# Optimization experiments

Measured on AMD Instinct MI355X. Metric: run time of the kernel, lower is better.

The kernel has to match this reference:

```python
import jax, jax.numpy as jnp
import numpy as np

B, T, C = 16, 1024, 1024
H = 4          # wshare
K = 31         # kernel_size


def setup_inputs() -> dict:
    key = jax.random.key(0)
    ks = jax.random.split(key, 8)
    s = 1.0 / np.sqrt(C)
    return {
        "query": jax.random.normal(ks[0], (B, T, C), jnp.float32),
        "key_t": jax.random.normal(ks[1], (B, T, C), jnp.float32),   # unused, API compat
        "value": jax.random.normal(ks[2], (B, T, C), jnp.float32),   # unused, API compat
        "mask": jnp.ones((B, 1, T), jnp.int32),
        "W1": jax.random.uniform(ks[3], (2 * C, C), jnp.float32, -s, s),
        "b1": jnp.zeros((2 * C,), jnp.float32),
        "W2": jax.random.uniform(ks[4], (C, C), jnp.float32, -s, s),
        "b2": jnp.zeros((C,), jnp.float32),
        "conv_w": jax.random.uniform(ks[5], (H, K), jnp.float32, 0.0, 1.0),
        "bias": jnp.zeros((C,), jnp.float32),
    }


def reference(query, key_t, value, mask, W1, b1, W2, b2, conv_w, bias):
    # linear1 + GLU: (B,T,C) -> (B,T,2C) -> (B,T,C)
    x = query @ W1.T + b1
    a, g = jnp.split(x, 2, axis=-1)
    x = a * jax.nn.sigmoid(g)
    # (B,T,C) -> (B,C,T) -> (B*C/H, H, T); channel c uses shared kernel c % H
    x = jnp.transpose(x, (0, 2, 1)).reshape(B * C // H, H, T)
    # softmax-normalized shared kernels (H,K); dropout_rate=0 (eval)
    w = jax.nn.softmax(conv_w, axis=-1)
    y = jax.lax.conv_general_dilated(
        x, w[:, None, :], window_strides=(1,), padding=[(K // 2, K // 2)],
        feature_group_count=H, dimension_numbers=("NCH", "OIH", "NCH"))
    x = y.reshape(B, C, T) + bias[None, :, None]
    x = jnp.transpose(x, (0, 2, 1))               # (B,T,C)
    # padding mask: (B,1,T) -> transpose(-1,-2) -> (B,T,1), zero masked frames
    m = jnp.transpose(mask, (0, 2, 1))
    x = jnp.where(m == 0, 0.0, x)
    return x @ W2.T + b2
```

## Files before the change

kernel.cpp:

```cpp
#include <hip/hip_runtime.h>

typedef __attribute__((ext_vector_type(8))) __bf16 bf16x8;
typedef __attribute__((ext_vector_type(4))) __bf16 bf16x4;
typedef __attribute__((ext_vector_type(4))) float  f32x4;
typedef __attribute__((ext_vector_type(4))) float  float4v;

#define DEV static __device__ __forceinline__

DEV void gload_lds16(const void* g, void* l) {
  __builtin_amdgcn_global_load_lds(
      (const __attribute__((address_space(1))) void*)g,
      (__attribute__((address_space(3))) void*)l, 16, 0, 0);
}

__global__ void prep_all_kernel(const float* __restrict__ q, const float* __restrict__ W1,
                                const float* __restrict__ W2, const float* __restrict__ cw,
                                const float* __restrict__ b1,
                                __bf16* __restrict__ qb, __bf16* __restrict__ w1p,
                                __bf16* __restrict__ w2b,
                                float* __restrict__ swm, float* __restrict__ b1p) {
  const int blk = blockIdx.x;
  const int tid = threadIdx.x;
  if (blk < 2048) {
    int i = blk * 256 + tid;
#pragma unroll 8
    for (int it = 0; it < 8; ++it, i += 524288) {
      float4v v = ((const float4v*)q)[i];
      bf16x4 o;
#pragma unroll
      for (int j = 0; j < 4; ++j) o[j] = (__bf16)v[j];
      ((bf16x4*)qb)[i] = o;
    }
  } else if (blk < 3072) {
    const int r   = (blk - 2048) * 2 + (tid >> 7);
    const int col = (tid & 127) * 8;
    const int g  = r >> 8, p = r & 255;
    const int wn = p >> 6, jj = (p >> 4) & 3, c16 = p & 15;
    const int ch = g * 128 + wn * 32 + (jj & 1) * 16 + c16;
    const int src = ch + (jj >= 2 ? 1024 : 0);
    const float* ptr = W1 + (long)src * 1024 + col;
    float4v v0 = *(const float4v*)ptr;
    float4v v1 = *(const float4v*)(ptr + 4);
    bf16x8 o;
#pragma unroll
    for (int j = 0; j < 4; ++j) { o[j] = (__bf16)v0[j]; o[4 + j] = (__bf16)v1[j]; }
    *(bf16x8*)(w1p + (long)r * 1024 + col) = o;
  } else if (blk < 3328) {
    int i = (blk - 3072) * 256 + tid;
#pragma unroll 4
    for (int it = 0; it < 4; ++it, i += 65536) {
      float4v v = ((const float4v*)W2)[i];
      bf16x4 o;
#pragma unroll
      for (int j = 0; j < 4; ++j) o[j] = (__bf16)v[j];
      ((bf16x4*)w2b)[i] = o;
    }
  } else {
    if (tid < 4) {
      const int h = tid;
      float m = cw[h * 31];
#pragma unroll
      for (int k = 1; k < 31; ++k) m = fmaxf(m, cw[h * 31 + k]);
      float e[31];
      float s = 0.f;
#pragma unroll
      for (int k = 0; k < 31; ++k) {
        e[k] = __expf(cw[h * 31 + k] - m);
        s += e[k];
      }
      float inv = 1.f / s;
#pragma unroll
      for (int k = 0; k < 31; ++k) swm[h * 31 + k] = e[k] * inv;
    }
    for (int i = tid; i < 2048; i += 256) {
      const int g = i >> 8, p = i & 255;
      const int wn = p >> 6, jj = (p >> 4) & 3, c16 = p & 15;
      const int ch = g * 128 + wn * 32 + (jj & 1) * 16 + c16;
      b1p[i] = b1[ch + (jj >= 2 ? 1024 : 0)];
    }
  }
}

template <int MODE>
DEV void gemm_body(const __bf16* __restrict__ A, const __bf16* __restrict__ Bw,
                   const float* __restrict__ bias, void* __restrict__ Cout,
                   int M, int N, int K, int ntn) {
  __shared__ __align__(16) __bf16 Al[3 * 16384];
  __shared__ __align__(16) __bf16 Bl[2 * 16384];

  const int tid  = threadIdx.x;
  const int lane = tid & 63;
  const int w    = tid >> 6;
  const int wm = w >> 2, wn = w & 3;

  const int nwg = gridDim.x;
  const int cpx = nwg >> 3;
  const int bid = blockIdx.x;
  const int wgid = (bid & 7) * cpx + (bid >> 3);
  const int m0 = (wgid / ntn) * 256;
  const int n0 = (wgid % ntn) * 256;

  const int NT = K >> 6;

  const int scolE = ((((tid & 7) * 16) ^ (((tid >> 3) & 7) << 4)) >> 1);
  const __bf16* __restrict__ Abase = A + (long)m0 * K;
  const __bf16* __restrict__ Bbase = Bw + (long)n0 * K;

  const int l15 = lane & 15;
  const int xk  = (l15 & 7) << 4;
  const int a0  = l15 * 128 + (((lane >> 4) * 16) ^ xk);
  const int a1  = l15 * 128 + ((((lane >> 4) * 16) + 64) ^ xk);
  const int bq  = (wn & 1) * 8192;
  const int b0  = bq + a0;
  const int b1r = bq + a1;

  f32x4 acc[8][4];
#pragma unroll
  for (int i = 0; i < 8; ++i)
#pragma unroll
    for (int j = 0; j < 4; ++j) {
      acc[i][j][0] = 0.f; acc[i][j][1] = 0.f;
      acc[i][j][2] = 0.f; acc[i][j][3] = 0.f;
    }
  bf16x8 af[8], bf[8];

#define STAGEG(base, groff, ktc, dst)                                             \
  {                                                                               \
    const __bf16* _s = (base) + (long)((groff) + (tid >> 3)) * K + (ktc) + scolE; \
    gload_lds16(_s, (dst) + tid * 8);                                             \
    gload_lds16(_s + (long)64 * K, (dst) + 4096 + tid * 8);                       \
  }

#define PH_MID()                                     \
  __builtin_amdgcn_s_barrier();                      \
  asm volatile("s_waitcnt lgkmcnt(0)" ::: "memory"); \
  __builtin_amdgcn_s_setprio(1);

#define PH_ENDN()                                    \
  __builtin_amdgcn_s_setprio(0);                     \
  __builtin_amdgcn_s_barrier();

#define PH_END4()                                    \
  __builtin_amdgcn_s_setprio(0);                     \
  asm volatile("s_waitcnt vmcnt(4)" ::: "memory");   \
  __builtin_amdgcn_s_barrier();

#define RDA(IB, G)                                                    \
  _Pragma("unroll") for (int i2 = 0; i2 < 4; ++i2) {                  \
    af[i2 * 2 + 0] = *(const bf16x8*)((G) + ((IB) + i2) * 2048 + a0); \
    af[i2 * 2 + 1] = *(const bf16x8*)((G) + ((IB) + i2) * 2048 + a1); \
  }
#define RDB(JB, G)                                                                \
  _Pragma("unroll") for (int j2 = 0; j2 < 2; ++j2) {                              \
    bf[(JB) * 2 + j2 * 2 + 0] = *(const bf16x8*)((G) + ((JB) + j2) * 2048 + b0);  \
    bf[(JB) * 2 + j2 * 2 + 1] = *(const bf16x8*)((G) + ((JB) + j2) * 2048 + b1r); \
  }

#define MMQ(IB, JB)                                                           \
  _Pragma("unroll") for (int i2 = 0; i2 < 4; ++i2)                            \
  _Pragma("unroll") for (int j2 = 0; j2 < 2; ++j2)                            \
  _Pragma("unroll") for (int kk = 0; kk < 2; ++kk)                            \
      acc[(IB) + i2][(JB) + j2] = __builtin_amdgcn_mfma_f32_16x16x32_bf16(    \
          af[i2 * 2 + kk], bf[(JB) * 2 + j2 * 2 + kk], acc[(IB) + i2][(JB) + j2], 0, 0, 0);

  __bf16* aRd = Al;
  __bf16* aNx = Al + 16384;
  __bf16* aSt = Al + 32768;
  __bf16* bRd = Bl;
  __bf16* bSt = Bl + 16384;

  STAGEG(Abase, 0,   0, aRd);
  STAGEG(Abase, 128, 0, aRd + 8192);
  STAGEG(Bbase, 0,   0, bRd);
  STAGEG(Bbase, 128, 0, bRd + 8192);
  {
    const int k1 = (1 < NT ? 1 : NT - 1) * 64;
    STAGEG(Abase, 0,   k1, aNx);
    STAGEG(Abase, 128, k1, aNx + 8192);
  }
  asm volatile("s_waitcnt vmcnt(4)" ::: "memory");
  __builtin_amdgcn_s_barrier();

#pragma unroll 1
  for (int t = 0; t < NT; ++t) {
    const int kB = ((t + 1 < NT) ? t + 1 : NT - 1) * 64;
    const int kA = ((t + 2 < NT) ? t + 2 : NT - 1) * 64;
    const char* aG = (const char*)aRd + wm * 16384;
    const char* bG = (const char*)bRd + (wn >> 1) * 16384;
    RDA(0, aG); RDB(0, bG);
    STAGEG(Bbase, 0,   kB, bSt);
    STAGEG(Bbase, 128, kB, bSt + 8192);
    PH_MID(); MMQ(0, 0); PH_ENDN();
    RDB(2, bG);
    STAGEG(Abase, 0,   kA, aSt);
    STAGEG(Abase, 128, kA, aSt + 8192);
    PH_MID(); MMQ(0, 2); PH_ENDN();
    RDA(4, aG);
    PH_MID(); MMQ(4, 0); PH_ENDN();
    PH_MID(); MMQ(4, 2); PH_END4();
    __bf16* ta = aRd; aRd = aNx; aNx = aSt; aSt = ta;
    __bf16* tb = bRd; bRd = bSt; bSt = tb;
  }

  asm volatile("s_waitcnt vmcnt(0)" ::: "memory");

  const int crow = (lane >> 4) * 4;
  const int ccol = lane & 15;
  if (MODE == 0) {
    __builtin_amdgcn_s_barrier();
    float* wa = (float*)Al + w * 1088;
    const int rr = lane >> 4;
    const int cf = (lane & 15) * 4;
#pragma unroll
    for (int i = 0; i < 8; ++i) {
#pragma unroll
      for (int j = 0; j < 4; ++j) {
        const int ncol = n0 + wn * 64 + j * 16 + ccol;
        const float bv = bias[ncol];
#pragma unroll
        for (int r = 0; r < 4; ++r)
          wa[(crow + r) * 68 + j * 16 + ccol] = acc[i][j][r] + bv;
      }
#pragma unroll
      for (int s = 0; s < 4; ++s) {
        const int row = s * 4 + rr;
        const int gr = m0 + wm * 128 + i * 16 + row;
        *(float4v*)((float*)Cout + (long)gr * N + n0 + wn * 64 + cf) =
            *(const f32x4*)(wa + row * 68 + cf);
      }
    }
  } else {
    __builtin_amdgcn_s_barrier();
    __bf16* wa = (__bf16*)Al + w * 640;
    const int chbase = (n0 >> 1) + wn * 32;
    const int rr = lane >> 2, c8 = (lane & 3) * 8;
#pragma unroll
    for (int i = 0; i < 8; ++i) {
#pragma unroll
      for (int j = 0; j < 2; ++j) {
        const int na = n0 + wn * 64 + j * 16 + ccol;
        const float bva = bias[na];
        const float bvg = bias[na + 32];
#pragma unroll
        for (int r = 0; r < 4; ++r) {
          float a = acc[i][j][r] + bva;
          float gv = acc[i][j + 2][r] + bvg;
          float res = a * __builtin_amdgcn_rcpf(1.f + __expf(-gv));
          wa[(crow + r) * 40 + j * 16 + ccol] = (__bf16)res;
        }
      }
      bf16x8 v = *(const bf16x8*)(wa + rr * 40 + c8);
      const int gr = m0 + wm * 128 + i * 16 + rr;
      *(bf16x8*)((__bf16*)Cout + (long)gr * (N >> 1) + chbase + c8) = v;
    }
  }
#undef STAGEG
#undef PH_MID
#undef PH_ENDN
#undef PH_END4
#undef RDA
#undef RDB
#undef MMQ
}

__global__ __launch_bounds__(512, 1)
void gemm1_glu_kernel(const __bf16* __restrict__ A, const __bf16* __restrict__ Bw,
                      const float* __restrict__ bias, void* __restrict__ Cout,
                      int M, int N, int K, int ntn) {
  gemm_body<1>(A, Bw, bias, Cout, M, N, K, ntn);
}

__global__ __launch_bounds__(512, 1)
void gemm2_out_kernel(const __bf16* __restrict__ A, const __bf16* __restrict__ Bw,
                      const float* __restrict__ bias, void* __restrict__ Cout,
                      int M, int N, int K, int ntn) {
  gemm_body<0>(A, Bw, bias, Cout, M, N, K, ntn);
}

__global__ __launch_bounds__(256, 2)
void conv_kernel(const __bf16* __restrict__ Yin, const float* __restrict__ Wsm,
                 const float* __restrict__ bias, const int* __restrict__ mask,
                 __bf16* __restrict__ Y) {
  const int b  = blockIdx.z;
  const int t0 = blockIdx.y * 64;
  const int c0 = blockIdx.x * 128;
  __shared__ float sgT[128][128];
  __shared__ float swl[124];
  const int tid = threadIdx.x;
  if (tid < 124) swl[tid] = Wsm[tid];

  for (int i = tid; i < 2048; i += 256) {
    const int ttl = i & 127;
    const int cg  = i >> 7;
    if (ttl < 94) {
      const int t = t0 - 15 + ttl;
      float v[8];
      if (t >= 0 && t < 1024) {
        bf16x8 a8 = *(const bf16x8*)(Yin + ((long)(b * 1024 + t)) * 1024 + c0 + cg * 8);
#pragma unroll
        for (int j = 0; j < 8; ++j) v[j] = (float)a8[j];
      } else {
#pragma unroll
        for (int j = 0; j < 8; ++j) v[j] = 0.f;
      }
      const int q = ttl >> 2, e = ttl & 3;
#pragma unroll
      for (int j = 0; j < 8; ++j) {
        const int c = cg * 8 + j;
        sgT[c][((q ^ ((c & 7) << 2)) << 2) + e] = v[j];
      }
    }
  }
  __syncthreads();

  const int cc = tid & 127;
  const int th = tid >> 7;
  const int c  = c0 + cc;
  const float* wrow = swl + (c & 3) * 31;
  const float bv = bias[c];
  float acc[32];
#pragma unroll
  for (int u = 0; u < 32; ++u) acc[u] = bv;
  const int key = (cc & 7) << 2;
#pragma unroll
  for (int qi = 0; qi < 16; ++qi) {
    const int q = th * 8 + qi;
    const f32x4 w4 = *(const f32x4*)&sgT[cc][(q ^ key) << 2];
#pragma unroll
    for (int j = 0; j < 4; ++j) {
      const int rl = qi * 4 + j;
#pragma unroll
      for (int u = 0; u < 32; ++u) {
        const int k = rl - u;
        if (k >= 0 && k < 31) acc[u] += w4[j] * wrow[k];
      }
    }
  }
  const long yb = (long)b * 1024 * 1024;
#pragma unroll
  for (int u = 0; u < 32; ++u) {
    const int gt = t0 + th * 32 + u;
    float v = acc[u];
    if (mask[b * 1024 + gt] == 0) v = 0.f;
    Y[yb + (long)gt * 1024 + c] = (__bf16)v;
  }
}

extern "C" void kernel_launch(void* const* d_in, const int* in_sizes, int n_in,
                              void* d_out, int out_size, void* d_ws, size_t ws_size,
                              hipStream_t stream) {
  const float* q    = (const float*)d_in[0];
  const int*   mask = (const int*)d_in[3];
  const float* W1   = (const float*)d_in[4];
  const float* b1   = (const float*)d_in[5];
  const float* W2   = (const float*)d_in[6];
  const float* b2   = (const float*)d_in[7];
  const float* cw   = (const float*)d_in[8];
  const float* bias = (const float*)d_in[9];

  char* ws = (char*)d_ws;
  __bf16* q_bf  = (__bf16*)(ws);
  __bf16* w1p   = (__bf16*)(ws + (32u << 20));
  __bf16* w2_bf = (__bf16*)(ws + (36u << 20));
  float*  swm   = (float*)(ws + (38u << 20));
  float*  b1p   = (float*)(ws + (38u << 20) + 4096);
  __bf16* y     = (__bf16*)d_out;
  __bf16* yc    = q_bf;

  prep_all_kernel<<<3329, 256, 0, stream>>>(q, W1, W2, cw, b1,
                                            q_bf, w1p, w2_bf, swm, b1p);

  gemm1_glu_kernel<<<512, 512, 0, stream>>>(q_bf, w1p, b1p, (void*)y,
                                            16384, 2048, 1024, 8);
  conv_kernel<<<dim3(8, 16, 16), 256, 0, stream>>>(y, swm, bias, mask, yc);
  gemm2_out_kernel<<<256, 512, 0, stream>>>(yc, w2_bf, b2, d_out,
                                            16384, 1024, 1024, 4);
}
```

Before: 157.3 us.

## Fuse fp32-to-bf16 conversion of query into GEMM1 A-tile loading

Drops the separate pass in the prep kernel that converted the fp32 query tensor to bf16. GEMM1 now loads fp32 A tiles into registers, converts them to bf16 and writes them to LDS inside the pipelined K-loop, replacing the direct global-to-LDS loads. This removes a full read and write of the 64MB query tensor, at the cost of twice the global bytes per A tile in GEMM1, extra registers, and a full vmcnt(0) wait inside each iteration that may reduce load/compute overlap.

After: 159.1 us. Within noise of the previous version (+1.1%).

```diff
diff --git a/kernel.cpp b/kernel.cpp
--- a/kernel.cpp
+++ b/kernel.cpp
@@ -13,26 +13,14 @@
       (__attribute__((address_space(3))) void*)l, 16, 0, 0);
 }
 
-__global__ void prep_all_kernel(const float* __restrict__ q, const float* __restrict__ W1,
-                                const float* __restrict__ W2, const float* __restrict__ cw,
-                                const float* __restrict__ b1,
-                                __bf16* __restrict__ qb, __bf16* __restrict__ w1p,
-                                __bf16* __restrict__ w2b,
+__global__ void prep_all_kernel(const float* __restrict__ W1, const float* __restrict__ W2,
+                                const float* __restrict__ cw, const float* __restrict__ b1,
+                                __bf16* __restrict__ w1p, __bf16* __restrict__ w2b,
                                 float* __restrict__ swm, float* __restrict__ b1p) {
   const int blk = blockIdx.x;
   const int tid = threadIdx.x;
-  if (blk < 2048) {
-    int i = blk * 256 + tid;
-#pragma unroll 8
-    for (int it = 0; it < 8; ++it, i += 524288) {
-      float4v v = ((const float4v*)q)[i];
-      bf16x4 o;
-#pragma unroll
-      for (int j = 0; j < 4; ++j) o[j] = (__bf16)v[j];
-      ((bf16x4*)qb)[i] = o;
-    }
-  } else if (blk < 3072) {
-    const int r   = (blk - 2048) * 2 + (tid >> 7);
+  if (blk < 1024) {
+    const int r   = blk * 2 + (tid >> 7);
     const int col = (tid & 127) * 8;
     const int g  = r >> 8, p = r & 255;
     const int wn = p >> 6, jj = (p >> 4) & 3, c16 = p & 15;
@@ -45,8 +33,8 @@
 #pragma unroll
     for (int j = 0; j < 4; ++j) { o[j] = (__bf16)v0[j]; o[4 + j] = (__bf16)v1[j]; }
     *(bf16x8*)(w1p + (long)r * 1024 + col) = o;
-  } else if (blk < 3328) {
-    int i = (blk - 3072) * 256 + tid;
+  } else if (blk < 1280) {
+    int i = (blk - 1024) * 256 + tid;
 #pragma unroll 4
     for (int it = 0; it < 4; ++it, i += 65536) {
       float4v v = ((const float4v*)W2)[i];
@@ -82,7 +70,7 @@
 }
 
 template <int MODE>
-DEV void gemm_body(const __bf16* __restrict__ A, const __bf16* __restrict__ Bw,
+DEV void gemm_body(const void* __restrict__ A, const __bf16* __restrict__ Bw,
                    const float* __restrict__ bias, void* __restrict__ Cout,
                    int M, int N, int K, int ntn) {
   __shared__ __align__(16) __bf16 Al[3 * 16384];
@@ -103,7 +91,8 @@
   const int NT = K >> 6;
 
   const int scolE = ((((tid & 7) * 16) ^ (((tid >> 3) & 7) << 4)) >> 1);
-  const __bf16* __restrict__ Abase = A + (long)m0 * K;
+  const __bf16* __restrict__ Abase = (const __bf16*)A + (long)m0 * K;
+  const float*  __restrict__ Afb   = (const float*)A + (long)m0 * K;
   const __bf16* __restrict__ Bbase = Bw + (long)n0 * K;
 
   const int l15 = lane & 15;
@@ -123,12 +112,31 @@
       acc[i][j][2] = 0.f; acc[i][j][3] = 0.f;
     }
   bf16x8 af[8], bf[8];
+  float4v rA[8];
 
 #define STAGEG(base, groff, ktc, dst)                                             \
   {                                                                               \
     const __bf16* _s = (base) + (long)((groff) + (tid >> 3)) * K + (ktc) + scolE; \
     gload_lds16(_s, (dst) + tid * 8);                                             \
     gload_lds16(_s + (long)64 * K, (dst) + 4096 + tid * 8);                       \
+  }
+
+#define ALOADQ(ktc)                                                               \
+  _Pragma("unroll") for (int gg = 0; gg < 2; ++gg)                                \
+  _Pragma("unroll") for (int hh = 0; hh < 2; ++hh) {                              \
+    const float* _s = Afb + (long)(gg * 128 + hh * 64 + (tid >> 3)) * K + (ktc) + scolE; \
+    rA[(gg * 2 + hh) * 2 + 0] = *(const float4v*)_s;                              \
+    rA[(gg * 2 + hh) * 2 + 1] = *(const float4v*)(_s + 4);                        \
+  }
+#define AWRITEQ(dst)                                                              \
+  _Pragma("unroll") for (int gg = 0; gg < 2; ++gg)                                \
+  _Pragma("unroll") for (int hh = 0; hh < 2; ++hh) {                              \
+    bf16x8 o;                                                                     \
+    _Pragma("unroll") for (int e = 0; e < 4; ++e) {                               \
+      o[e]     = (__bf16)rA[(gg * 2 + hh) * 2 + 0][e];                            \
+      o[4 + e] = (__bf16)rA[(gg * 2 + hh) * 2 + 1][e];                            \
+    }                                                                             \
+    *(bf16x8*)((dst) + gg * 8192 + hh * 4096 + tid * 8) = o;                      \
   }
 
 #define PH_MID()                                     \
@@ -169,16 +177,24 @@
   __bf16* bRd = Bl;
   __bf16* bSt = Bl + 16384;
 
-  STAGEG(Abase, 0,   0, aRd);
-  STAGEG(Abase, 128, 0, aRd + 8192);
   STAGEG(Bbase, 0,   0, bRd);
   STAGEG(Bbase, 128, 0, bRd + 8192);
-  {
-    const int k1 = (1 < NT ? 1 : NT - 1) * 64;
+  const int k1 = (1 < NT ? 1 : NT - 1) * 64;
+  if (MODE == 1) {
+    ALOADQ(0);
+    asm volatile("s_waitcnt vmcnt(0)" ::: "memory");
+    AWRITEQ(aRd);
+    ALOADQ(k1);
+    asm volatile("s_waitcnt vmcnt(0)" ::: "memory");
+    AWRITEQ(aNx);
+    asm volatile("s_waitcnt lgkmcnt(0)" ::: "memory");
+  } else {
+    STAGEG(Abase, 0,   0, aRd);
+    STAGEG(Abase, 128, 0, aRd + 8192);
     STAGEG(Abase, 0,   k1, aNx);
     STAGEG(Abase, 128, k1, aNx + 8192);
-  }
-  asm volatile("s_waitcnt vmcnt(4)" ::: "memory");
+    asm volatile("s_waitcnt vmcnt(0)" ::: "memory");
+  }
   __builtin_amdgcn_s_barrier();
 
 #pragma unroll 1
@@ -192,12 +208,18 @@
     STAGEG(Bbase, 128, kB, bSt + 8192);
     PH_MID(); MMQ(0, 0); PH_ENDN();
     RDB(2, bG);
-    STAGEG(Abase, 0,   kA, aSt);
-    STAGEG(Abase, 128, kA, aSt + 8192);
+    if (MODE == 1) { ALOADQ(kA); }
+    else { STAGEG(Abase, 0, kA, aSt); STAGEG(Abase, 128, kA, aSt + 8192); }
     PH_MID(); MMQ(0, 2); PH_ENDN();
     RDA(4, aG);
     PH_MID(); MMQ(4, 0); PH_ENDN();
-    PH_MID(); MMQ(4, 2); PH_END4();
+    if (MODE == 1) {
+      asm volatile("s_waitcnt vmcnt(0)" ::: "memory");
+      AWRITEQ(aSt);
+      PH_MID(); MMQ(4, 2); PH_ENDN();
+    } else {
+      PH_MID(); MMQ(4, 2); PH_END4();
+    }
     __bf16* ta = aRd; aRd = aNx; aNx = aSt; aSt = ta;
     __bf16* tb = bRd; bRd = bSt; bSt = tb;
   }
@@ -255,6 +277,8 @@
     }
   }
 #undef STAGEG
+#undef ALOADQ
+#undef AWRITEQ
 #undef PH_MID
 #undef PH_ENDN
 #undef PH_END4
@@ -264,14 +288,14 @@
 }
 
 __global__ __launch_bounds__(512, 1)
-void gemm1_glu_kernel(const __bf16* __restrict__ A, const __bf16* __restrict__ Bw,
+void gemm1_glu_kernel(const void* __restrict__ A, const __bf16* __restrict__ Bw,
                       const float* __restrict__ bias, void* __restrict__ Cout,
                       int M, int N, int K, int ntn) {
   gemm_body<1>(A, Bw, bias, Cout, M, N, K, ntn);
 }
 
 __global__ __launch_bounds__(512, 1)
-void gemm2_out_kernel(const __bf16* __restrict__ A, const __bf16* __restrict__ Bw,
+void gemm2_out_kernel(const void* __restrict__ A, const __bf16* __restrict__ Bw,
                       const float* __restrict__ bias, void* __restrict__ Cout,
                       int M, int N, int K, int ntn) {
   gemm_body<0>(A, Bw, bias, Cout, M, N, K, ntn);
@@ -359,20 +383,18 @@
   const float* bias = (const float*)d_in[9];
 
   char* ws = (char*)d_ws;
-  __bf16* q_bf  = (__bf16*)(ws);
+  __bf16* yc    = (__bf16*)(ws);
   __bf16* w1p   = (__bf16*)(ws + (32u << 20));
   __bf16* w2_bf = (__bf16*)(ws + (36u << 20));
   float*  swm   = (float*)(ws + (38u << 20));
   float*  b1p   = (float*)(ws + (38u << 20) + 4096);
   __bf16* y     = (__bf16*)d_out;
-  __bf16* yc    = q_bf;
-
-  prep_all_kernel<<<3329, 256, 0, stream>>>(q, W1, W2, cw, b1,
-                                            q_bf, w1p, w2_bf, swm, b1p);
-
-  gemm1_glu_kernel<<<512, 512, 0, stream>>>(q_bf, w1p, b1p, (void*)y,
+
+  prep_all_kernel<<<1281, 256, 0, stream>>>(W1, W2, cw, b1, w1p, w2_bf, swm, b1p);
+
+  gemm1_glu_kernel<<<512, 512, 0, stream>>>((const void*)q, w1p, b1p, (void*)y,
                                             16384, 2048, 1024, 8);
   conv_kernel<<<dim3(8, 16, 16), 256, 0, stream>>>(y, swm, bias, mask, yc);
-  gemm2_out_kernel<<<256, 512, 0, stream>>>(yc, w2_bf, b2, d_out,
+  gemm2_out_kernel<<<256, 512, 0, stream>>>((const void*)yc, w2_bf, b2, d_out,
                                             16384, 1024, 1024, 4);
 }
```
